# Kernel tuning notes

Hardware: AMD Instinct MI355X
Metric: run time of the kernel (lower is better)

Reference implementation:

```python
import jax, jax.numpy as jnp
import numpy as np

B, S, D, H = 2, 4096, 1024, 16
DK = D // H


def setup_inputs() -> dict:
    key = jax.random.key(0)
    ks = jax.random.split(key, 8)
    scale = 1.0 / np.sqrt(D)
    return {
        "q": jax.random.normal(ks[0], (B, S, D), dtype=jnp.float32),
        "k": jax.random.normal(ks[1], (B, S, D), dtype=jnp.float32),
        "v": jax.random.normal(ks[2], (B, S, D), dtype=jnp.float32),
        "mask": jax.random.randint(ks[3], (1, 1, S, S), 0, 2, dtype=jnp.int32),
        "w_q": jax.random.normal(ks[4], (D, D), dtype=jnp.float32) * scale,
        "w_k": jax.random.normal(ks[5], (D, D), dtype=jnp.float32) * scale,
        "w_v": jax.random.normal(ks[6], (D, D), dtype=jnp.float32) * scale,
        "w_o": jax.random.normal(ks[7], (D, D), dtype=jnp.float32) * scale,
    }


def reference(q, k, v, mask, w_q, w_k, w_v, w_o):
    # torch Linear(bias=False): y = x @ W.T
    def proj_split(x, w):
        y = jnp.einsum("bsd,ed->bse", x, w)  # [B,S,D]
        return y.reshape(x.shape[0], -1, H, DK).transpose(0, 2, 1, 3)  # [B,H,S,dk]

    Q = proj_split(q, w_q)
    K = proj_split(k, w_k)
    V = proj_split(v, w_v)

    scores = jnp.einsum("bhqd,bhkd->bhqk", Q, K) / jnp.sqrt(jnp.float32(DK))
    scores = jnp.where(mask == 0, jnp.float32(-1e9), scores)
    attn = jax.nn.softmax(scores, axis=-1)  # dropout p=0 -> identity
    ctx = jnp.einsum("bhqk,bhkd->bhqd", attn, V)  # [B,H,S,dk]
    ctx = ctx.transpose(0, 2, 1, 3).reshape(q.shape[0], -1, D)  # [B,S,D]
    return jnp.einsum("bsd,ed->bse", ctx, w_o)
```

## Files before the change

### kernel.cpp

```cpp
#include <hip/hip_runtime.h>
#include <math.h>
#include <stdint.h>

constexpr int B = 2, S = 4096, D = 1024, H = 16, DK = 64;
constexpr int M_TOT = B * S;

typedef __attribute__((ext_vector_type(8))) short bf16x8;
typedef __attribute__((ext_vector_type(4))) float f32x4;
typedef __attribute__((ext_vector_type(4))) uint32_t u32x4;
typedef unsigned short u16;

__device__ inline u16 f2bf(float f) {
    uint32_t u = __builtin_bit_cast(uint32_t, f);
    u += 0x7fffu + ((u >> 16) & 1u);
    return (u16)(u >> 16);
}

__device__ inline u16 f2bf_hw(float f) {
    __bf16 h = (__bf16)f;
    return __builtin_bit_cast(u16, h);
}

__device__ inline void gl2lds16(const void* g, void* l) {
    __builtin_amdgcn_global_load_lds((const __attribute__((address_space(1))) void*)g,
                                     (__attribute__((address_space(3))) void*)l, 16, 0, 0);
}

__global__ __launch_bounds__(256) void conv_bf16(const float* __restrict__ s0, const float* __restrict__ s1,
                                                 const float* __restrict__ s2, const float* __restrict__ s3,
                                                 u16* __restrict__ d0, u16* __restrict__ d1,
                                                 u16* __restrict__ d2, u16* __restrict__ d3, int n) {
    const float* s; u16* d;
    switch (blockIdx.y) {
        case 0: s = s0; d = d0; break;
        case 1: s = s1; d = d1; break;
        case 2: s = s2; d = d2; break;
        default: s = s3; d = d3; break;
    }
    const int i = (blockIdx.x * 256 + threadIdx.x) * 4;
    if (i < n) {
        float4 v = *(const float4*)(s + i);
        ushort4 o;
        o.x = f2bf(v.x); o.y = f2bf(v.y); o.z = f2bf(v.z); o.w = f2bf(v.w);
        *(ushort4*)(d + i) = o;
    }
}

__global__ __launch_bounds__(256) void mask_pack(const int* __restrict__ m, uint32_t* __restrict__ out) {
    const int i = blockIdx.x * 256 + threadIdx.x;
    const int base = i * 32;
    uint32_t b = 0;
#pragma unroll
    for (int j = 0; j < 32; ++j) b |= (m[base + j] != 0 ? 1u : 0u) << j;
    out[i] = b;
}

template <typename OutT>
__global__ __launch_bounds__(256) void gemm_bt(const u16* __restrict__ X, const u16* __restrict__ Wm,
                                               OutT* __restrict__ Y, int M, int N, int K, float oscale) {
    __shared__ u16 As[128 * 64];
    __shared__ u16 Bs[128 * 64];
    const int tid = threadIdx.x;
    const int lane = tid & 63;
    const int wave = tid >> 6;
    const int l15 = lane & 15;
    const int quad = lane >> 4;
    const int i0 = blockIdx.x * 128;
    const int j0 = blockIdx.y * 128;
    const int wm = wave & 1, wn = wave >> 1;
    const int lr = lane >> 3;
    const int lc = (lane & 7) * 8;

    f32x4 zero = {0.f, 0.f, 0.f, 0.f};
    f32x4 acc[4][4];
#pragma unroll
    for (int a = 0; a < 4; ++a)
#pragma unroll
        for (int b2 = 0; b2 < 4; ++b2) acc[a][b2] = zero;

    for (int k0 = 0; k0 < K; k0 += 64) {
#pragma unroll
        for (int c = 0; c < 4; ++c) {
            const int ch = wave * 4 + c;
            const int row = ch * 8 + lr;
            gl2lds16(X + (size_t)(i0 + row) * K + k0 + lc, &As[ch * 512]);
            gl2lds16(Wm + (size_t)(j0 + row) * K + k0 + lc, &Bs[ch * 512]);
        }
        __syncthreads();
        bf16x8 af[4][2];
#pragma unroll
        for (int mt = 0; mt < 4; ++mt)
#pragma unroll
            for (int ks = 0; ks < 2; ++ks)
                af[mt][ks] = *(const bf16x8*)&As[(wm * 64 + mt * 16 + l15) * 64 + ks * 32 + quad * 8];
#pragma unroll
        for (int nt = 0; nt < 4; ++nt) {
#pragma unroll
            for (int ks = 0; ks < 2; ++ks) {
                bf16x8 bfr = *(const bf16x8*)&Bs[(wn * 64 + nt * 16 + l15) * 64 + ks * 32 + quad * 8];
#pragma unroll
                for (int mt = 0; mt < 4; ++mt)
                    acc[mt][nt] = __builtin_amdgcn_mfma_f32_16x16x32_bf16(af[mt][ks], bfr, acc[mt][nt], 0, 0, 0);
            }
        }
        __syncthreads();
    }
#pragma unroll
    for (int mt = 0; mt < 4; ++mt) {
#pragma unroll
        for (int r = 0; r < 4; ++r) {
            const int gi = i0 + wm * 64 + mt * 16 + quad * 4 + r;
#pragma unroll
            for (int nt = 0; nt < 4; ++nt) {
                const int gj = j0 + wn * 64 + nt * 16 + l15;
                const float v = acc[mt][nt][r] * oscale;
                if constexpr (sizeof(OutT) == 2) {
                    Y[(size_t)gi * N + gj] = (OutT)f2bf(v);
                } else {
                    Y[(size_t)gi * N + gj] = v;
                }
            }
        }
    }
}

__global__ __launch_bounds__(256) void attn_mfma(const u16* __restrict__ Qb, const u16* __restrict__ Kb,
                                                 const u16* __restrict__ Vt,
                                                 const uint64_t* __restrict__ mask64,
                                                 u16* __restrict__ ctx) {
    __shared__ u16 Ks[64 * 64];
    __shared__ u16 Vs[64 * 64];
    const int tid = threadIdx.x;
    const int lane = tid & 63;
    const int wave = tid >> 6;
    const int l15 = lane & 15;
    const int quad = lane >> 4;
    const int q0 = blockIdx.x * 128;
    const int bh = blockIdx.y;
    const int bb = bh >> 4, hh = bh & 15;
    const int mbase = bb * S;
    const int e0 = hh * DK;
    const int r7 = l15 & 7;

    const int srow = tid >> 2;
    const int scb = tid & 3;

    bf16x8 aq[2][2];
#pragma unroll
    for (int mi = 0; mi < 2; ++mi) {
        const u16* qrow = Qb + (size_t)(mbase + q0 + wave * 32 + mi * 16 + l15) * D + e0;
        aq[mi][0] = *(const bf16x8*)(qrow + quad * 8);
        aq[mi][1] = *(const bf16x8*)(qrow + 32 + quad * 8);
    }

    f32x4 O[2][4];
    f32x4 Ol[2];
#pragma unroll
    for (int mi = 0; mi < 2; ++mi) {
        Ol[mi] = (f32x4){0.f, 0.f, 0.f, 0.f};
#pragma unroll
        for (int dt = 0; dt < 4; ++dt) O[mi][dt] = (f32x4){0.f, 0.f, 0.f, 0.f};
    }

    bf16x8 ONES;
#pragma unroll
    for (int i = 0; i < 8; ++i) ONES[i] = (short)0x3F80;

    const uint64_t* mrow[2];
#pragma unroll
    for (int mi = 0; mi < 2; ++mi)
        mrow[mi] = mask64 + (size_t)(q0 + wave * 32 + mi * 16 + l15) * (S / 64);

    for (int kt = 0; kt < S / 64; ++kt) {
        const int kb = kt * 64;
#pragma unroll
        for (int it = 0; it < 2; ++it) {
            const int cb = scb + it * 4;
            const int phys = cb ^ (srow & 7);
            const bf16x8 kvv = *(const bf16x8*)(Kb + (size_t)(mbase + kb + srow) * D + e0 + cb * 8);
            *(bf16x8*)&Ks[srow * 64 + phys * 8] = kvv;
            const int k0v = 32 * (cb >> 2) + 4 * (cb & 3);
            const u16* vsrc = Vt + (size_t)(e0 + srow) * M_TOT + mbase + kb + k0v;
            const uint64_t va = *(const uint64_t*)(vsrc);
            const uint64_t vb = *(const uint64_t*)(vsrc + 16);
            *(uint64_t*)&Vs[srow * 64 + phys * 8] = va;
            *(uint64_t*)&Vs[srow * 64 + phys * 8 + 4] = vb;
        }
        __syncthreads();

        bf16x8 kf[4][2];
#pragma unroll
        for (int nt = 0; nt < 4; ++nt) {
            kf[nt][0] = *(const bf16x8*)&Ks[(nt * 16 + l15) * 64 + (quad ^ r7) * 8];
            kf[nt][1] = *(const bf16x8*)&Ks[(nt * 16 + l15) * 64 + ((quad + 4) ^ r7) * 8];
        }

        bf16x8 ap[2][2];
#pragma unroll
        for (int mi = 0; mi < 2; ++mi) {
            f32x4 sa[4];
#pragma unroll
            for (int nt = 0; nt < 4; ++nt) {
                f32x4 c = {0.f, 0.f, 0.f, 0.f};
                c = __builtin_amdgcn_mfma_f32_16x16x32_bf16(kf[nt][0], aq[mi][0], c, 0, 0, 0);
                c = __builtin_amdgcn_mfma_f32_16x16x32_bf16(kf[nt][1], aq[mi][1], c, 0, 0, 0);
                sa[nt] = c;
            }
            const uint64_t mw = mrow[mi][kt];
            const uint32_t mlo = (uint32_t)(mw >> (quad * 4));
            const uint32_t mhi = (uint32_t)(mw >> (quad * 4 + 32));
            uint32_t pk[4][2];
#pragma unroll
            for (int nt = 0; nt < 4; ++nt) {
                const uint32_t mx = (nt < 2) ? mlo : mhi;
                float p[4];
#pragma unroll
                for (int r = 0; r < 4; ++r) {
                    const float e = __builtin_amdgcn_exp2f(sa[nt][r]);
                    p[r] = ((mx >> ((nt & 1) * 16 + r)) & 1u) ? e : 0.f;
                }
                pk[nt][0] = (uint32_t)f2bf_hw(p[0]) | ((uint32_t)f2bf_hw(p[1]) << 16);
                pk[nt][1] = (uint32_t)f2bf_hw(p[2]) | ((uint32_t)f2bf_hw(p[3]) << 16);
            }
            const u32x4 w0 = {pk[0][0], pk[0][1], pk[1][0], pk[1][1]};
            const u32x4 w1 = {pk[2][0], pk[2][1], pk[3][0], pk[3][1]};
            ap[mi][0] = __builtin_bit_cast(bf16x8, w0);
            ap[mi][1] = __builtin_bit_cast(bf16x8, w1);
        }

#pragma unroll
        for (int mi = 0; mi < 2; ++mi) {
            Ol[mi] = __builtin_amdgcn_mfma_f32_16x16x32_bf16(ap[mi][0], ONES, Ol[mi], 0, 0, 0);
            Ol[mi] = __builtin_amdgcn_mfma_f32_16x16x32_bf16(ap[mi][1], ONES, Ol[mi], 0, 0, 0);
        }
#pragma unroll
        for (int dt = 0; dt < 4; ++dt) {
            const bf16x8 bv0 = *(const bf16x8*)&Vs[(dt * 16 + l15) * 64 + (quad ^ r7) * 8];
            const bf16x8 bv1 = *(const bf16x8*)&Vs[(dt * 16 + l15) * 64 + ((quad + 4) ^ r7) * 8];
#pragma unroll
            for (int mi = 0; mi < 2; ++mi) {
                O[mi][dt] = __builtin_amdgcn_mfma_f32_16x16x32_bf16(ap[mi][0], bv0, O[mi][dt], 0, 0, 0);
                O[mi][dt] = __builtin_amdgcn_mfma_f32_16x16x32_bf16(ap[mi][1], bv1, O[mi][dt], 0, 0, 0);
            }
        }
        __syncthreads();
    }

#pragma unroll
    for (int mi = 0; mi < 2; ++mi) {
#pragma unroll
        for (int r = 0; r < 4; ++r) {
            const float inv = 1.f / Ol[mi][r];
            const int gm = mbase + q0 + wave * 32 + mi * 16 + quad * 4 + r;
#pragma unroll
            for (int dt = 0; dt < 4; ++dt)
                ctx[(size_t)gm * D + e0 + dt * 16 + l15] = f2bf(O[mi][dt][r] * inv);
        }
    }
}

extern "C" void kernel_launch(void* const* d_in, const int* in_sizes, int n_in,
                              void* d_out, int out_size, void* d_ws, size_t ws_size,
                              hipStream_t stream) {
    (void)in_sizes; (void)n_in; (void)out_size; (void)ws_size;
    const float* q = (const float*)d_in[0];
    const float* k = (const float*)d_in[1];
    const float* v = (const float*)d_in[2];
    const int* msk = (const int*)d_in[3];
    const float* w_q = (const float*)d_in[4];
    const float* w_k = (const float*)d_in[5];
    const float* w_v = (const float*)d_in[6];
    const float* w_o = (const float*)d_in[7];
    float* out = (float*)d_out;

    const size_t MB = 1u << 20;
    char* w = (char*)d_ws;
    u16* qb   = (u16*)(w + 0 * MB);
    u16* kb   = (u16*)(w + 16 * MB);
    u16* vb   = (u16*)(w + 32 * MB);
    u16* wqb  = (u16*)(w + 48 * MB);
    u16* wkb  = (u16*)(w + 50 * MB);
    u16* wvb  = (u16*)(w + 52 * MB);
    u16* wob  = (u16*)(w + 54 * MB);
    uint64_t* maskb = (uint64_t*)(w + 56 * MB);
    u16* Qf   = (u16*)(w + 58 * MB);
    u16* Kf   = (u16*)(w + 74 * MB);
    u16* Vtf  = (u16*)(w + 90 * MB);
    u16* ctxb = (u16*)(w + 106 * MB);

    const float SCL2 = 0.18033688011112042f;

    dim3 blk(256);
    conv_bf16<<<dim3(8192, 3), blk, 0, stream>>>(q, k, v, q, qb, kb, vb, qb, M_TOT * D);
    conv_bf16<<<dim3(1024, 4), blk, 0, stream>>>(w_q, w_k, w_v, w_o, wqb, wkb, wvb, wob, D * D);
    mask_pack<<<dim3(S * S / 32 / 256), blk, 0, stream>>>(msk, (uint32_t*)maskb);

    gemm_bt<u16><<<dim3(M_TOT / 128, D / 128), blk, 0, stream>>>(qb, wqb, Qf, M_TOT, D, D, SCL2);
    gemm_bt<u16><<<dim3(M_TOT / 128, D / 128), blk, 0, stream>>>(kb, wkb, Kf, M_TOT, D, D, 1.0f);
    gemm_bt<u16><<<dim3(D / 128, M_TOT / 128), blk, 0, stream>>>(wvb, vb, Vtf, D, M_TOT, D, 1.0f);

    attn_mfma<<<dim3(S / 128, B * H), blk, 0, stream>>>(Qf, Kf, Vtf, maskb, ctxb);

    gemm_bt<float><<<dim3(M_TOT / 128, D / 128), blk, 0, stream>>>(ctxb, wob, out, M_TOT, D, D, 1.0f);
}
```

Measured before the change: 535.3 us.

## Register-prefetch next K/V tile, remap blocks per XCD, add MFMA priority hints

The attention loop now loads the next K, V and mask tile into registers before computing on the current one, ping-ponging between two register stages. This hides global-load latency behind MFMA work. Block indices are remapped so that blocks of the same batch-head land on the same XCD, which should improve L2 reuse of K/V. s_setprio is raised around the MFMA sections. The cost is higher register pressure, and the barrier structure relies on raw s_barrier and lgkmcnt waits rather than __syncthreads.

Measured after the change: 516.1 us. 3.6% less time.

```diff
diff --git a/kernel.cpp b/kernel.cpp
--- a/kernel.cpp
+++ b/kernel.cpp
@@ -124,6 +124,12 @@
     }
 }
 
+struct KVStage {
+    bf16x8 rk[2];
+    uint64_t rva[2], rvb[2];
+    uint64_t rm[2];
+};
+
 __global__ __launch_bounds__(256) void attn_mfma(const u16* __restrict__ Qb, const u16* __restrict__ Kb,
                                                  const u16* __restrict__ Vt,
                                                  const uint64_t* __restrict__ mask64,
@@ -135,8 +141,13 @@
     const int wave = tid >> 6;
     const int l15 = lane & 15;
     const int quad = lane >> 4;
-    const int q0 = blockIdx.x * 128;
-    const int bh = blockIdx.y;
+
+    const int bid = blockIdx.y * (S / 128) + blockIdx.x;
+    const int xcd = bid & 7;
+    const int loc = bid >> 3;
+    const int bh = xcd * 4 + (loc >> 5);
+    const int q0 = (loc & 31) * 128;
+
     const int bb = bh >> 4, hh = bh & 15;
     const int mbase = bb * S;
     const int e0 = hh * DK;
@@ -171,23 +182,33 @@
     for (int mi = 0; mi < 2; ++mi)
         mrow[mi] = mask64 + (size_t)(q0 + wave * 32 + mi * 16 + l15) * (S / 64);
 
-    for (int kt = 0; kt < S / 64; ++kt) {
+    auto LOADT = [&](KVStage& st, int kt) {
         const int kb = kt * 64;
+#pragma unroll
+        for (int it = 0; it < 2; ++it) {
+            const int cb = scb + it * 4;
+            st.rk[it] = *(const bf16x8*)(Kb + (size_t)(mbase + kb + srow) * D + e0 + cb * 8);
+            const int k0v = 32 * (cb >> 2) + 4 * (cb & 3);
+            const u16* vsrc = Vt + (size_t)(e0 + srow) * M_TOT + mbase + kb + k0v;
+            st.rva[it] = *(const uint64_t*)(vsrc);
+            st.rvb[it] = *(const uint64_t*)(vsrc + 16);
+        }
+#pragma unroll
+        for (int mi = 0; mi < 2; ++mi) st.rm[mi] = mrow[mi][kt];
+    };
+
+    auto WRITET = [&](const KVStage& st) {
 #pragma unroll
         for (int it = 0; it < 2; ++it) {
             const int cb = scb + it * 4;
             const int phys = cb ^ (srow & 7);
-            const bf16x8 kvv = *(const bf16x8*)(Kb + (size_t)(mbase + kb + srow) * D + e0 + cb * 8);
-            *(bf16x8*)&Ks[srow * 64 + phys * 8] = kvv;
-            const int k0v = 32 * (cb >> 2) + 4 * (cb & 3);
-            const u16* vsrc = Vt + (size_t)(e0 + srow) * M_TOT + mbase + kb + k0v;
-            const uint64_t va = *(const uint64_t*)(vsrc);
-            const uint64_t vb = *(const uint64_t*)(vsrc + 16);
-            *(uint64_t*)&Vs[srow * 64 + phys * 8] = va;
-            *(uint64_t*)&Vs[srow * 64 + phys * 8 + 4] = vb;
-        }
-        __syncthreads();
-
+            *(bf16x8*)&Ks[srow * 64 + phys * 8] = st.rk[it];
+            *(uint64_t*)&Vs[srow * 64 + phys * 8] = st.rva[it];
+            *(uint64_t*)&Vs[srow * 64 + phys * 8 + 4] = st.rvb[it];
+        }
+    };
+
+    auto COMPUTE = [&](const KVStage& st) {
         bf16x8 kf[4][2];
 #pragma unroll
         for (int nt = 0; nt < 4; ++nt) {
@@ -199,6 +220,7 @@
 #pragma unroll
         for (int mi = 0; mi < 2; ++mi) {
             f32x4 sa[4];
+            __builtin_amdgcn_s_setprio(1);
 #pragma unroll
             for (int nt = 0; nt < 4; ++nt) {
                 f32x4 c = {0.f, 0.f, 0.f, 0.f};
@@ -206,7 +228,8 @@
                 c = __builtin_amdgcn_mfma_f32_16x16x32_bf16(kf[nt][1], aq[mi][1], c, 0, 0, 0);
                 sa[nt] = c;
             }
-            const uint64_t mw = mrow[mi][kt];
+            __builtin_amdgcn_s_setprio(0);
+            const uint64_t mw = st.rm[mi];
             const uint32_t mlo = (uint32_t)(mw >> (quad * 4));
             const uint32_t mhi = (uint32_t)(mw >> (quad * 4 + 32));
             uint32_t pk[4][2];
@@ -228,6 +251,7 @@
             ap[mi][1] = __builtin_bit_cast(bf16x8, w1);
         }
 
+        __builtin_amdgcn_s_setprio(1);
 #pragma unroll
         for (int mi = 0; mi < 2; ++mi) {
             Ol[mi] = __builtin_amdgcn_mfma_f32_16x16x32_bf16(ap[mi][0], ONES, Ol[mi], 0, 0, 0);
@@ -243,7 +267,27 @@
                 O[mi][dt] = __builtin_amdgcn_mfma_f32_16x16x32_bf16(ap[mi][1], bv1, O[mi][dt], 0, 0, 0);
             }
         }
-        __syncthreads();
+        __builtin_amdgcn_s_setprio(0);
+    };
+
+    KVStage stA, stB;
+    LOADT(stA, 0);
+    for (int kt = 0; kt < S / 64; kt += 2) {
+        LOADT(stB, kt + 1);
+        __builtin_amdgcn_s_barrier();
+        WRITET(stA);
+        asm volatile("s_waitcnt lgkmcnt(0)" ::: "memory");
+        __builtin_amdgcn_s_barrier();
+        __builtin_amdgcn_sched_barrier(0);
+        COMPUTE(stA);
+
+        if (kt + 2 < S / 64) LOADT(stA, kt + 2);
+        __builtin_amdgcn_s_barrier();
+        WRITET(stB);
+        asm volatile("s_waitcnt lgkmcnt(0)" ::: "memory");
+        __builtin_amdgcn_s_barrier();
+        __builtin_amdgcn_sched_barrier(0);
+        COMPUTE(stB);
     }
 
 #pragma unroll
```
